# Kernel tuning notes

Measured on AMD Instinct MI355X. Metric: run time of the kernel, lower is better.

Reference implementation:

```python
import jax, jax.numpy as jnp
from jax import lax
import numpy as np

EPS = 1e-7          # BCE clamp
SMOOTH = 1.0        # Dice smoothing
INT_INF = jnp.int32(2**31 - 1)


def _bce_dice(p, t):
    """BCE + Dice loss (standard BCEDiceLoss): p, t float32 in [0,1]."""
    pc = jnp.clip(p, EPS, 1.0 - EPS)
    bce = -jnp.mean(t * jnp.log(pc) + (1.0 - t) * jnp.log1p(-pc))
    inter = jnp.sum(p * t)
    dice = 1.0 - (2.0 * inter + SMOOTH) / (jnp.sum(p) + jnp.sum(t) + SMOOTH)
    return bce + dice


def _ccl(mask):
    """4-connected component labeling per batch image.
    mask: [B,H,W] bool. Returns (labels, init_labels) int32; 0 = background.
    Iterative min-label propagation to a fixpoint (lax.while_loop)."""
    B, H, W = mask.shape
    init = jnp.where(mask, jnp.arange(1, B * H * W + 1, dtype=jnp.int32).reshape(B, H, W), 0)

    def step(lab):
        big = jnp.where(mask, lab, INT_INF)
        pad_h = jnp.full((B, 1, W), INT_INF, jnp.int32)
        pad_w = jnp.full((B, H, 1), INT_INF, jnp.int32)
        up    = jnp.concatenate([big[:, 1:, :], pad_h], axis=1)
        down  = jnp.concatenate([pad_h, big[:, :-1, :]], axis=1)
        left  = jnp.concatenate([big[:, :, 1:], pad_w], axis=2)
        right = jnp.concatenate([pad_w, big[:, :, :-1]], axis=2)
        m = jnp.minimum(big, jnp.minimum(jnp.minimum(up, down), jnp.minimum(left, right)))
        return jnp.where(mask, m, 0)

    def cond(c):
        return c[1]

    def body(c):
        new = step(c[0])
        return (new, jnp.any(new != c[0]))

    lab, _ = lax.while_loop(cond, body, (init, jnp.array(True)))
    return lab, init


def _forward(pred_out, target_mask, num_target_classes):
    f32 = jnp.float32
    B, C, H, W = pred_out.shape
    pred_masks = jnp.argmax(pred_out, axis=1)      # [B,H,W] int
    tm = target_mask[:, 0]                         # [B,H,W] int

    # background-vs-background BCEDice term
    res = _bce_dice((pred_masks == 0).astype(f32), (tm == 0).astype(f32))

    ph = jnp.zeros((B, H, W), f32)    # pred_placeholder
    pho = jnp.zeros((B, H, W), f32)   # pred_placeholder_out
    last_i = jnp.int32(1)

    # fixed loop over predicted classes (torch loops over unique values;
    # here: loop 1..C-1 gated by presence so absent classes are no-ops)
    for v in range(1, C):
        cur = pred_masks == v                       # class-v mask
        present = jnp.any(cur)
        lab, init = _ccl(cur)
        # number of connected components = pixels that kept their seed label
        n_comp = jnp.sum((lab == init) & cur).astype(jnp.int32)
        has_bg = jnp.any(~cur).astype(jnp.int32)    # 0 in cur_uniq?
        # sum_c (c_mask + last_i) over components == cur + n_comp*last_i everywhere
        inc = cur.astype(f32) + (n_comp * last_i).astype(f32)
        ph = jnp.where(present, ph + inc, ph)
        pho = jnp.where(cur, pred_out[:, v], pho)
        last_i = last_i + jnp.where(present, n_comp + has_bg, 0)

    # loop over nonzero target ids (bounded by num_target_classes), gated by presence
    for t in range(1, num_target_classes):
        target_m = tm == t
        present = jnp.any(target_m)
        n = jnp.sum(target_m)
        # torch.median(ph[target_m]): lower median of masked values
        vals = jnp.where(target_m.reshape(-1), ph.reshape(-1), jnp.inf)
        med = jnp.sort(vals)[jnp.maximum((n - 1) // 2, 0)]
        tm_f = target_m.astype(f32)
        contrib = _bce_dice(pho * (ph == med).astype(f32), tm_f)
        extra = jnp.sum(pho * ((ph != med) & target_m).astype(f32)) / jnp.maximum(n, 1).astype(f32)
        res = res + jnp.where(present, contrib + extra, 0.0)

    # len(torch.unique(target_mask)) with values in [0, num_target_classes)
    n_unique = jnp.sum(jnp.stack([jnp.any(tm == t) for t in range(num_target_classes)]).astype(jnp.int32))
    return res / (2 * n_unique + 1).astype(f32)


def setup_inputs() -> dict:
    key = jax.random.key(0)
    k1, k2 = jax.random.split(key)
    B, C, H, W = 8, 5, 768, 768
    pred_out = jax.random.uniform(k1, (B, C, H, W), dtype=jnp.float32)
    target_mask = jax.random.randint(k2, (B, 1, H, W), 0, 4, dtype=jnp.int32)
    return {"pred_out": pred_out, "target_mask": target_mask, "num_target_classes": 4}


def reference(pred_out, target_mask, num_target_classes):
    return _forward(pred_out, target_mask, num_target_classes)
```

## Files before the change

kernel.cpp:

```cpp
#include <hip/hip_runtime.h>
#include <stdint.h>
#include <math.h>

#define B_ 8
#define C_ 5
#define H_ 768
#define W_ 768
#define HW_ (H_*W_)
#define HWq (HW_/4)
#define NPIX (B_*HW_)
#define TB 8
#define INVAL 0xFFFFFFFFu
#define LN2F 0.69314718056f
#define BIASF 16.2f
#define TILE 32
#define TPR 24
#define TPC 24
#define NTILES (B_*TPR*TPC)
#define NPT 128
#define NNODES (NTILES*NPT)
#define SEAMS_PER_IMG (23*768)
#define NB_HALF (B_*SEAMS_PER_IMG)
#define NB_TOT (2*NB_HALF)
#define SEAMBLK (NB_TOT/256)
#define NCOPY 32

typedef unsigned long long ull;

static __device__ __forceinline__ unsigned pload(const unsigned* P, unsigned i) {
  return __hip_atomic_load(&P[i], __ATOMIC_RELAXED, __HIP_MEMORY_SCOPE_AGENT);
}
static __device__ unsigned findRootG(unsigned* P, unsigned i) {
  unsigned p = pload(P, i);
  if (p == i) return i;
  unsigned gp = pload(P, p);
  while (p != gp) {
    __hip_atomic_store(&P[i], gp, __ATOMIC_RELAXED, __HIP_MEMORY_SCOPE_AGENT);
    i = p; p = gp; gp = pload(P, p);
  }
  return p;
}
static __device__ bool uniteG(unsigned* P, unsigned a, unsigned b) {
  a = findRootG(P, a);
  b = findRootG(P, b);
  while (a != b) {
    if (a < b) { unsigned t = a; a = b; b = t; }
    unsigned old = atomicCAS(&P[a], a, b);
    if (old == a) return true;
    a = findRootG(P, old);
    b = findRootG(P, b);
  }
  return false;
}
static __device__ __forceinline__ unsigned ploadL(const unsigned* P, unsigned i) {
  return __hip_atomic_load(&P[i], __ATOMIC_RELAXED, __HIP_MEMORY_SCOPE_WORKGROUP);
}
static __device__ unsigned findRootL(const unsigned* P, unsigned i) {
  unsigned p = ploadL(P, i) & 0xFFFFu;
  while (p != i) { i = p; p = ploadL(P, i) & 0xFFFFu; }
  return i;
}
static __device__ void uniteL(unsigned* P, unsigned a, unsigned b) {
  a = findRootL(P, a);
  b = findRootL(P, b);
  while (a != b) {
    if (a < b) { unsigned t = a; a = b; b = t; }
    unsigned old = atomicCAS(&P[a], 0xFFFF0000u | a, 0xFFFF0000u | b);
    if (old == (0xFFFF0000u | a)) return;
    a = findRootL(P, old & 0xFFFFu);
    b = findRootL(P, b);
  }
}

__global__ __launch_bounds__(256, 8) void k_stats_ccl(
    const float* __restrict__ pred, const int* __restrict__ tgt,
    unsigned short* __restrict__ border, unsigned* __restrict__ P2,
    unsigned* __restrict__ rootcnt, double* __restrict__ sp,
    unsigned* __restrict__ ctrl)
{
  __shared__ ull h[NCOPY][41];
  __shared__ unsigned lab[TILE*TILE];
  __shared__ unsigned lclsw[TILE*TILE/4];
  __shared__ unsigned s_rt[4];
  unsigned char* lcls = (unsigned char*)lclsw;

  for (int i = threadIdx.x; i < NCOPY*41; i += 256) (&h[0][0])[i] = 0ull;
  if (threadIdx.x < 4) s_rt[threadIdx.x] = 0u;
  if (threadIdx.x < NPT) {
    unsigned n = (unsigned)blockIdx.x * NPT + threadIdx.x;
    P2[n] = n;
  }
  if (blockIdx.x == 0 && threadIdx.x == 0) ctrl[8] = 0u;
  __syncthreads();

  const int cp = threadIdx.x & (NCOPY - 1);
  int blk = blockIdx.x;
  int b = blk / (TPR*TPC);
  int rem = blk - b * (TPR*TPC);
  int trow = rem / TPR;
  int ty0 = trow * TILE;
  int tx0 = (rem - trow * TPR) * TILE;

  unsigned pk = 0u;
  {
    const int baseq = ty0 * (W_/4) + (tx0 >> 2);
    const int qrow = threadIdx.x >> 3, qcol = threadIdx.x & 7;
    const int o = qrow * (W_/4) + qcol;
    const float4* pp = (const float4*)pred + (size_t)b * (C_*HWq) + baseq + o;
    float4 a0 = pp[0];
    float4 a1 = pp[HWq];
    float4 a2 = pp[2*HWq];
    float4 a3 = pp[3*HWq];
    float4 a4 = pp[4*HWq];
    int4 t4 = ((const int4*)tgt)[(size_t)b * HWq + baseq + o];
#pragma unroll
    for (int j = 0; j < 4; ++j) {
      float v0 = ((const float*)&a0)[j];
      float v1 = ((const float*)&a1)[j];
      float v2 = ((const float*)&a2)[j];
      float v3 = ((const float*)&a3)[j];
      float v4 = ((const float*)&a4)[j];
      int tt = ((const int*)&t4)[j];
      float best = v0; int bc = 0;
      if (v1 > best) { best = v1; bc = 1; }
      if (v2 > best) { best = v2; bc = 2; }
      if (v3 > best) { best = v3; bc = 3; }
      if (v4 > best) { best = v4; bc = 4; }
      unsigned tu = (unsigned)tt; if (tu >= TB) tu = TB - 1;
      ull w;
      if (bc) {
        float pc = fminf(fmaxf(best, 1e-7f), 1.0f - 1e-7f);
        float l2p = __log2f(pc);
        float l2m = __log2f(1.0f - pc);
        float logit = (l2p - l2m) * LN2F;
        float mag   = -l2m * LN2F;
        w = (1ull << 57)
          | ((ull)__float2uint_rn(best * 4096.0f) << 38)
          | ((ull)__float2uint_rn((logit + BIASF) * 64.0f) << 20)
          | (ull)__float2uint_rn(mag * 64.0f);
      } else {
        w = 1ull << 57;
      }
      atomicAdd(&h[cp][(int)tu * C_ + bc], w);
      pk |= ((unsigned)bc) << (8 * j);
    }
    lclsw[threadIdx.x] = pk;
  }
  __syncthreads();

  const int r = threadIdx.x >> 3, sub = threadIdx.x & 7;
  const int seg = r * TILE + sub * 4;
  unsigned Dw = (r < TILE-1) ? lclsw[threadIdx.x + 8] : 0u;
  unsigned rb = (sub < 7) ? (lclsw[threadIdx.x + 1] & 255u) : 0u;
  {
    uint4 lw;
    unsigned* lp = (unsigned*)&lw;
#pragma unroll
    for (int k = 0; k < 4; ++k) {
      int li = seg + k;
      unsigned c = (pk >> (8 * k)) & 255u;
      lp[k] = c ? (0xFFFF0000u | (unsigned)li) : INVAL;
    }
    *(uint4*)&lab[seg] = lw;
  }
  __syncthreads();

#pragma unroll
  for (int j = 0; j < 4; ++j) {
    unsigned c = (pk >> (8 * j)) & 255u;
    if (!c) continue;
    int li = seg + j;
    unsigned cr = (j < 3) ? ((pk >> (8 * (j + 1))) & 255u) : rb;
    if (cr == c) uniteL(lab, li, li + 1);
    if (((Dw >> (8 * j)) & 255u) == c) uniteL(lab, li, li + TILE);
  }
  __syncthreads();

  {
    uint4 lw = *(const uint4*)&lab[seg];
    const unsigned* lp = (const unsigned*)&lw;
#pragma unroll
    for (int k = 0; k < 4; ++k) {
      int li = seg + k;
      unsigned c = (pk >> (8 * k)) & 255u;
      if (c && (lp[k] & 0xFFFFu) == (unsigned)li) atomicAdd(&s_rt[c - 1], 1u);
    }
  }
  unsigned bc_c = 0, bc_rt = 0;
  if (threadIdx.x < NPT) {
    int bp = threadIdx.x;
    int tx, ty;
    if (bp < 32)       { ty = 0;       tx = bp; }
    else if (bp < 64)  { ty = TILE-1;  tx = bp - 32; }
    else if (bp < 96)  { tx = 0;       ty = bp - 64; }
    else               { tx = TILE-1;  ty = bp - 96; }
    int li = ty * TILE + tx;
    bc_c = lcls[li];
    if (bc_c) {
      bc_rt = findRootL(lab, (unsigned)li);
      atomicMin(&lab[bc_rt], ((unsigned)threadIdx.x << 16) | bc_rt);
    }
  }
  __syncthreads();
  if (threadIdx.x < NPT) {
    unsigned sub2 = bc_c ? (lab[bc_rt] >> 16) : 0u;
    border[blk * NPT + threadIdx.x] = (unsigned short)((bc_c << 8) | sub2);
  }
  if (threadIdx.x < 4) rootcnt[blk * 4 + threadIdx.x] = s_rt[threadIdx.x];
  if (threadIdx.x < 160) {
    int slot = threadIdx.x >> 2, comp = threadIdx.x & 3;
    double s = 0.0;
#pragma unroll
    for (int cc = 0; cc < NCOPY; ++cc) {
      ull w = h[cc][slot];
      if (comp == 0)      s += (double)(w >> 57);
      else if (comp == 1) s += (double)((w >> 38) & 0x7FFFFull) * (1.0/4096.0);
      else if (comp == 2) s += (double)((w >> 20) & 0x3FFFFull) * (1.0/64.0);
      else                s += (double)(w & 0x1FFFFull) * (1.0/64.0);
    }
    sp[(size_t)blk * 160 + threadIdx.x] = s;
  }
}

#define SH_CNT(t,c)   shist[((t)*C_+(c))*4 + 0]
#define SH_PRED(t,c)  shist[((t)*C_+(c))*4 + 1]
#define SH_LRAW(t,c)  shist[((t)*C_+(c))*4 + 2]
#define SH_MAG(t,c)   shist[((t)*C_+(c))*4 + 3]
__global__ __launch_bounds__(256) void k_seam_final(
    const unsigned short* __restrict__ border, unsigned* __restrict__ P2,
    const double* __restrict__ sp, const unsigned* __restrict__ rootcnt,
    unsigned* __restrict__ smcnt, ull* __restrict__ spf_u,
    unsigned* __restrict__ ctrl, const int* __restrict__ ntcp,
    float* __restrict__ out)
{
  __shared__ unsigned s_sub[4];
  __shared__ double red[256];
  __shared__ int s_last;
  __shared__ double shist[160];
  __shared__ double s_col[C_][3];
  __shared__ unsigned s_cnti[TB*C_];
  __shared__ unsigned s_ctot[C_];
  __shared__ unsigned s_nc[4], s_smg[4];
  __shared__ float s_ph[C_];
  __shared__ double s_term[TB];
  __shared__ int s_NT;
  __shared__ int s_nun;

  if (threadIdx.x < 4) s_sub[threadIdx.x] = 0u;
  __syncthreads();
  int idx = blockIdx.x * blockDim.x + threadIdx.x;
  {
    int tA, tB, pA, pB;
    if (idx < NB_HALF) {
      int b = idx / SEAMS_PER_IMG;
      int r = idx - b * SEAMS_PER_IMG;
      int seam = r / W_;
      int x = r - seam * W_;
      int tj = x >> 5, k = x & 31;
      tA = (b * TPC + seam) * TPR + tj;
      tB = tA + TPR;
      pA = tA * NPT + 32 + k;
      pB = tB * NPT + 0 + k;
    } else {
      int i2 = idx - NB_HALF;
      int b = i2 / SEAMS_PER_IMG;
      int r = i2 - b * SEAMS_PER_IMG;
      int seam = r / H_;
      int y = r - seam * H_;
      int ti = y >> 5, k = y & 31;
      tA = (b * TPC + ti) * TPR + seam;
      tB = tA + 1;
      pA = tA * NPT + 96 + k;
      pB = tB * NPT + 64 + k;
    }
    unsigned a16 = border[pA];
    unsigned b16 = border[pB];
    unsigned ca = a16 >> 8, cb = b16 >> 8;
    if (ca && ca == cb) {
      if (uniteG(P2, (unsigned)tA * NPT + (a16 & 255u),
                     (unsigned)tB * NPT + (b16 & 255u)))
        atomicAdd(&s_sub[ca - 1], 1u);
    }
  }
  if (blockIdx.x < 160) {
    double s = 0.0;
    for (int j = threadIdx.x; j < NTILES; j += 256) s += sp[(size_t)j * 160 + blockIdx.x];
    red[threadIdx.x] = s;
    __syncthreads();
    for (int off = 128; off; off >>= 1) {
      if (threadIdx.x < off) red[threadIdx.x] += red[threadIdx.x + off];
      __syncthreads();
    }
    if (threadIdx.x == 0)
      __hip_atomic_store(&spf_u[blockIdx.x], (ull)__double_as_longlong(red[0]),
                         __ATOMIC_RELAXED, __HIP_MEMORY_SCOPE_AGENT);
  }
  __syncthreads();
  if (threadIdx.x < 4)
    __hip_atomic_store(&smcnt[blockIdx.x * 4 + threadIdx.x], s_sub[threadIdx.x],
                       __ATOMIC_RELAXED, __HIP_MEMORY_SCOPE_AGENT);
  __syncthreads();
  if (threadIdx.x == 0) {
    unsigned old = __hip_atomic_fetch_add(&ctrl[8], 1u,
                     __ATOMIC_RELAXED, __HIP_MEMORY_SCOPE_AGENT);
    s_last = (old == (unsigned)(SEAMBLK - 1));
  }
  __syncthreads();
  if (!s_last) return;

  if (threadIdx.x < 160) {
    ull u = __hip_atomic_load(&spf_u[threadIdx.x],
              __ATOMIC_RELAXED, __HIP_MEMORY_SCOPE_AGENT);
    shist[threadIdx.x] = __longlong_as_double((long long)u);
  }
  if (threadIdx.x < 4) { s_nc[threadIdx.x] = 0u; s_smg[threadIdx.x] = 0u; }
  if (threadIdx.x < TB) s_term[threadIdx.x] = 0.0;
  if (threadIdx.x == 0) {
    int NT = ntcp[0];
    if (NT < 1) NT = 1;
    if (NT > TB) NT = TB;
    s_NT = NT;
  }
  __syncthreads();
  {
    unsigned a = 0;
    for (int j = threadIdx.x; j < NTILES * 4; j += 256) a += rootcnt[j];
    if (a) atomicAdd(&s_nc[threadIdx.x & 3], a);
  }
  {
    unsigned a = 0;
    for (int j = threadIdx.x; j < SEAMBLK * 4; j += 256)
      a += __hip_atomic_load(&smcnt[j], __ATOMIC_RELAXED, __HIP_MEMORY_SCOPE_AGENT);
    if (a) atomicAdd(&s_smg[threadIdx.x & 3], a);
  }
  __syncthreads();

  if (threadIdx.x < TB * C_) s_cnti[threadIdx.x] = (unsigned)llrint(shist[threadIdx.x * 4]);
  __syncthreads();

  if (threadIdx.x < C_) {
    int c = threadIdx.x;
    double sc = 0.0, sp2 = 0.0, sl = 0.0;
    unsigned ct = 0;
#pragma unroll
    for (int t = 0; t < TB; ++t) {
      sc += SH_CNT(t, c);
      sp2 += SH_PRED(t, c);
      sl += -SH_MAG(t, c);
      ct += s_cnti[t * C_ + c];
    }
    s_col[c][0] = sc; s_col[c][1] = sp2; s_col[c][2] = sl;
    s_ctot[c] = ct;
  }
  __syncthreads();

  if (threadIdx.x == 0) {
#pragma unroll
    for (int cc = 0; cc < C_; ++cc) {
      float ph = 0.0f;
      int li = 1;
#pragma unroll
      for (int v = 1; v < C_; ++v) {
        unsigned ncv = s_nc[v - 1] - s_smg[v - 1];
        if (s_ctot[v] > 0) {
          int prod = (int)(ncv * (unsigned)li);
          float sv = (float)prod;
          float inc = ((cc == v) ? 1.0f : 0.0f) + sv;
          ph = ph + inc;
          li = li + (int)ncv + ((s_ctot[v] < (unsigned)NPIX) ? 1 : 0);
        }
      }
      s_ph[cc] = ph;
    }
  }
  __syncthreads();

  const float EPSF = 1e-7f;
  const double L1 = (double)logf(1.0f - EPSF);
  const double M1 = (double)log1pf(-(1.0f - EPSF));
  const double L0 = (double)logf(EPSF);
  const double M0 = (double)log1pf(-EPSF);
  const double N = (double)NPIX;
  const double BIASD = (double)BIASF;
  const int NT = s_NT;

  if (threadIdx.x == 0) {
    double nt0 = 0;
#pragma unroll
    for (int c = 0; c < C_; ++c) nt0 += SH_CNT(0, c);
    double np1 = (double)s_ctot[0];
    double n11 = SH_CNT(0, 0);
    s_term[0] = -(n11*L1 + (nt0 - n11)*L0 + (np1 - n11)*M1 + (N - nt0 - np1 + n11)*M0) / N
                + 1.0 - (2.0*n11 + 1.0) / (np1 + nt0 + 1.0);
    int nun = 0;
    for (int t = 0; t < NT; ++t) {
      long long s = 0;
#pragma unroll
      for (int c = 0; c < C_; ++c) s += (long long)s_cnti[t * C_ + c];
      if (s) nun++;
    }
    s_nun = nun;
  } else if (threadIdx.x < (unsigned)NT) {
    int t = threadIdx.x;
    long long ntti = 0;
#pragma unroll
    for (int c = 0; c < C_; ++c) ntti += (long long)s_cnti[t * C_ + c];
    if (ntti != 0) {
      double ntt = 0;
#pragma unroll
      for (int c = 0; c < C_; ++c) ntt += SH_CNT(t, c);
      float pht[C_] = {s_ph[0], s_ph[1], s_ph[2], s_ph[3], s_ph[4]};
      int idx2[C_] = {0, 1, 2, 3, 4};
#pragma unroll
      for (int i = 1; i < C_; ++i)
        for (int j = i; j > 0 && pht[idx2[j]] < pht[idx2[j-1]]; --j) {
          int tmp = idx2[j]; idx2[j] = idx2[j-1]; idx2[j-1] = tmp;
        }
      long long k = (ntti - 1) / 2;
      float med = pht[idx2[C_ - 1]];
      long long cum = 0;
#pragma unroll
      for (int i = 0; i < C_; ++i) {
        cum += (long long)s_cnti[t * C_ + idx2[i]];
        if (cum > k) { med = pht[idx2[i]]; break; }
      }
      double A = 0, Bt = 0, inter = 0, sum_p = 0, ex = 0, nfg_t = 0, nfg_all = 0;
#pragma unroll
      for (int c = 1; c < C_; ++c) {
        double cnt_tc = SH_CNT(t, c);
        double mag_tc = SH_MAG(t, c);
        double spred_tc = SH_PRED(t, c);
        if (pht[c] == med) {
          double logit = SH_LRAW(t, c) - BIASD * cnt_tc;
          A += logit - mag_tc;
          inter += spred_tc;
          nfg_t += cnt_tc;
          nfg_all += s_col[c][0];
          sum_p += s_col[c][1];
          Bt += s_col[c][2] - (-mag_tc);
        } else {
          ex += spred_tc;
        }
      }
      double bce  = -(A + Bt + (ntt - nfg_t)*L0 + (N - ntt - (nfg_all - nfg_t))*M0) / N;
      double dice = 1.0 - (2.0*inter + 1.0) / (sum_p + ntt + 1.0);
      s_term[t] = bce + dice + ex / ntt;
    }
  }
  __syncthreads();
  if (threadIdx.x == 0) {
    double res = 0.0;
#pragma unroll
    for (int t = 0; t < TB; ++t) res += s_term[t];
    out[0] = (float)(res / (double)(2 * s_nun + 1));
  }
}

extern "C" void kernel_launch(void* const* d_in, const int* in_sizes, int n_in,
                              void* d_out, int out_size, void* d_ws, size_t ws_size,
                              hipStream_t stream) {
  const float* pred = (const float*)d_in[0];
  const int* tgt = (const int*)d_in[1];
  const int* ntc = (const int*)d_in[2];
  float* out = (float*)d_out;
  char* ws = (char*)d_ws;
  size_t off = 0;
  unsigned* ctrl = (unsigned*)(ws + off);        off += 16 * 4;
  ull* spf_u = (ull*)(ws + off);                 off += 160 * 8;
  double* sp = (double*)(ws + off);              off += (size_t)NTILES * 160 * 8;
  unsigned* P2 = (unsigned*)(ws + off);          off += (size_t)NNODES * 4;
  unsigned short* border = (unsigned short*)(ws + off); off += (size_t)NTILES * NPT * 2;
  unsigned* rootcnt = (unsigned*)(ws + off);     off += (size_t)NTILES * 4 * 4;
  unsigned* smcnt = (unsigned*)(ws + off);       off += (size_t)SEAMBLK * 4 * 4;

  hipLaunchKernelGGL(k_stats_ccl, dim3(NTILES), dim3(256), 0, stream,
                     pred, tgt, border, P2, rootcnt, sp, ctrl);
  hipLaunchKernelGGL(k_seam_final, dim3(SEAMBLK), dim3(256), 0, stream,
                     border, P2, sp, rootcnt, smcnt, spf_u, ctrl, ntc, out);
}
```

Baseline: 211.4 us.

## Replace per-tile partial-sum arrays with replicated global atomics and a separate final kernel

Per-tile double partial statistics (NTILES×160 doubles) and per-tile root counts are no longer written and later reduced. Each tile now does fixed-point integer atomic adds into a small replicated global accumulator. The seam kernel likewise atomically adds its counts into replicas, and a new single-block final kernel sums the replicas and resets them. This drops a large write-then-read reduction and the last-block detection, in exchange for atomic contention, a third kernel launch, and reliance on device globals being reset at the end of each call. NCOPY is also halved, which shrinks shared histogram memory.

After: 172.2 us. 18.5% less time.

```diff
diff --git a/kernel.cpp b/kernel.cpp
--- a/kernel.cpp
+++ b/kernel.cpp
@@ -23,9 +23,14 @@
 #define NB_HALF (B_*SEAMS_PER_IMG)
 #define NB_TOT (2*NB_HALF)
 #define SEAMBLK (NB_TOT/256)
-#define NCOPY 32
+#define NCOPY 16
+#define REPS 8
+#define REPC 64
 
 typedef unsigned long long ull;
+
+__device__ ull g_spu[REPS * 160];
+__device__ unsigned g_crep[REPC * 16];
 
 static __device__ __forceinline__ unsigned pload(const unsigned* P, unsigned i) {
   return __hip_atomic_load(&P[i], __ATOMIC_RELAXED, __HIP_MEMORY_SCOPE_AGENT);
@@ -74,9 +79,7 @@
 
 __global__ __launch_bounds__(256, 8) void k_stats_ccl(
     const float* __restrict__ pred, const int* __restrict__ tgt,
-    unsigned short* __restrict__ border, unsigned* __restrict__ P2,
-    unsigned* __restrict__ rootcnt, double* __restrict__ sp,
-    unsigned* __restrict__ ctrl)
+    unsigned short* __restrict__ border, unsigned* __restrict__ P2)
 {
   __shared__ ull h[NCOPY][41];
   __shared__ unsigned lab[TILE*TILE];
@@ -90,7 +93,6 @@
     unsigned n = (unsigned)blockIdx.x * NPT + threadIdx.x;
     P2[n] = n;
   }
-  if (blockIdx.x == 0 && threadIdx.x == 0) ctrl[8] = 0u;
   __syncthreads();
 
   const int cp = threadIdx.x & (NCOPY - 1);
@@ -206,46 +208,27 @@
     unsigned sub2 = bc_c ? (lab[bc_rt] >> 16) : 0u;
     border[blk * NPT + threadIdx.x] = (unsigned short)((bc_c << 8) | sub2);
   }
-  if (threadIdx.x < 4) rootcnt[blk * 4 + threadIdx.x] = s_rt[threadIdx.x];
+  if (threadIdx.x < 4 && s_rt[threadIdx.x])
+    atomicAdd(&g_crep[(blk & (REPC-1)) * 16 + threadIdx.x], s_rt[threadIdx.x]);
   if (threadIdx.x < 160) {
     int slot = threadIdx.x >> 2, comp = threadIdx.x & 3;
-    double s = 0.0;
+    ull fs = 0;
 #pragma unroll
     for (int cc = 0; cc < NCOPY; ++cc) {
       ull w = h[cc][slot];
-      if (comp == 0)      s += (double)(w >> 57);
-      else if (comp == 1) s += (double)((w >> 38) & 0x7FFFFull) * (1.0/4096.0);
-      else if (comp == 2) s += (double)((w >> 20) & 0x3FFFFull) * (1.0/64.0);
-      else                s += (double)(w & 0x1FFFFull) * (1.0/64.0);
-    }
-    sp[(size_t)blk * 160 + threadIdx.x] = s;
-  }
-}
-
-#define SH_CNT(t,c)   shist[((t)*C_+(c))*4 + 0]
-#define SH_PRED(t,c)  shist[((t)*C_+(c))*4 + 1]
-#define SH_LRAW(t,c)  shist[((t)*C_+(c))*4 + 2]
-#define SH_MAG(t,c)   shist[((t)*C_+(c))*4 + 3]
-__global__ __launch_bounds__(256) void k_seam_final(
-    const unsigned short* __restrict__ border, unsigned* __restrict__ P2,
-    const double* __restrict__ sp, const unsigned* __restrict__ rootcnt,
-    unsigned* __restrict__ smcnt, ull* __restrict__ spf_u,
-    unsigned* __restrict__ ctrl, const int* __restrict__ ntcp,
-    float* __restrict__ out)
+      if (comp == 0)      fs += (w >> 57);
+      else if (comp == 1) fs += (w >> 38) & 0x7FFFFull;
+      else if (comp == 2) fs += (w >> 20) & 0x3FFFFull;
+      else                fs += w & 0x1FFFFull;
+    }
+    if (fs) atomicAdd(&g_spu[(blk & (REPS-1)) * 160 + threadIdx.x], fs);
+  }
+}
+
+__global__ __launch_bounds__(256) void k_seam(const unsigned short* __restrict__ border,
+                                              unsigned* __restrict__ P2)
 {
   __shared__ unsigned s_sub[4];
-  __shared__ double red[256];
-  __shared__ int s_last;
-  __shared__ double shist[160];
-  __shared__ double s_col[C_][3];
-  __shared__ unsigned s_cnti[TB*C_];
-  __shared__ unsigned s_ctot[C_];
-  __shared__ unsigned s_nc[4], s_smg[4];
-  __shared__ float s_ph[C_];
-  __shared__ double s_term[TB];
-  __shared__ int s_NT;
-  __shared__ int s_nun;
-
   if (threadIdx.x < 4) s_sub[threadIdx.x] = 0u;
   __syncthreads();
   int idx = blockIdx.x * blockDim.x + threadIdx.x;
@@ -282,56 +265,49 @@
         atomicAdd(&s_sub[ca - 1], 1u);
     }
   }
-  if (blockIdx.x < 160) {
-    double s = 0.0;
-    for (int j = threadIdx.x; j < NTILES; j += 256) s += sp[(size_t)j * 160 + blockIdx.x];
-    red[threadIdx.x] = s;
-    __syncthreads();
-    for (int off = 128; off; off >>= 1) {
-      if (threadIdx.x < off) red[threadIdx.x] += red[threadIdx.x + off];
-      __syncthreads();
-    }
-    if (threadIdx.x == 0)
-      __hip_atomic_store(&spf_u[blockIdx.x], (ull)__double_as_longlong(red[0]),
-                         __ATOMIC_RELAXED, __HIP_MEMORY_SCOPE_AGENT);
-  }
-  __syncthreads();
-  if (threadIdx.x < 4)
-    __hip_atomic_store(&smcnt[blockIdx.x * 4 + threadIdx.x], s_sub[threadIdx.x],
-                       __ATOMIC_RELAXED, __HIP_MEMORY_SCOPE_AGENT);
-  __syncthreads();
-  if (threadIdx.x == 0) {
-    unsigned old = __hip_atomic_fetch_add(&ctrl[8], 1u,
-                     __ATOMIC_RELAXED, __HIP_MEMORY_SCOPE_AGENT);
-    s_last = (old == (unsigned)(SEAMBLK - 1));
-  }
-  __syncthreads();
-  if (!s_last) return;
+  __syncthreads();
+  if (threadIdx.x < 4 && s_sub[threadIdx.x])
+    atomicAdd(&g_crep[(blockIdx.x & (REPC-1)) * 16 + 4 + threadIdx.x], s_sub[threadIdx.x]);
+}
+
+#define SH_CNT(t,c)   shist[((t)*C_+(c))*4 + 0]
+#define SH_PRED(t,c)  shist[((t)*C_+(c))*4 + 1]
+#define SH_LRAW(t,c)  shist[((t)*C_+(c))*4 + 2]
+#define SH_MAG(t,c)   shist[((t)*C_+(c))*4 + 3]
+__global__ __launch_bounds__(256) void k_final(const int* __restrict__ ntcp,
+                                               float* __restrict__ out)
+{
+  __shared__ double shist[160];
+  __shared__ double s_col[C_][3];
+  __shared__ unsigned s_cnti[TB*C_];
+  __shared__ unsigned s_ctot[C_];
+  __shared__ unsigned s_nc[4], s_smg[4];
+  __shared__ float s_ph[C_];
+  __shared__ double s_term[TB];
+  __shared__ int s_NT;
+  __shared__ int s_nun;
 
   if (threadIdx.x < 160) {
-    ull u = __hip_atomic_load(&spf_u[threadIdx.x],
-              __ATOMIC_RELAXED, __HIP_MEMORY_SCOPE_AGENT);
-    shist[threadIdx.x] = __longlong_as_double((long long)u);
-  }
-  if (threadIdx.x < 4) { s_nc[threadIdx.x] = 0u; s_smg[threadIdx.x] = 0u; }
+    ull acc = 0;
+#pragma unroll
+    for (int rp = 0; rp < REPS; ++rp) acc += g_spu[rp * 160 + threadIdx.x];
+    int comp = threadIdx.x & 3;
+    shist[threadIdx.x] = (comp == 0) ? (double)acc
+                       : (comp == 1) ? (double)acc * (1.0/4096.0)
+                                     : (double)acc * (1.0/64.0);
+  }
+  if (threadIdx.x < 8) {
+    unsigned a = 0;
+    for (int rp = 0; rp < REPC; ++rp) a += g_crep[rp * 16 + threadIdx.x];
+    if (threadIdx.x < 4) s_nc[threadIdx.x] = a;
+    else                 s_smg[threadIdx.x - 4] = a;
+  }
   if (threadIdx.x < TB) s_term[threadIdx.x] = 0.0;
   if (threadIdx.x == 0) {
     int NT = ntcp[0];
     if (NT < 1) NT = 1;
     if (NT > TB) NT = TB;
     s_NT = NT;
-  }
-  __syncthreads();
-  {
-    unsigned a = 0;
-    for (int j = threadIdx.x; j < NTILES * 4; j += 256) a += rootcnt[j];
-    if (a) atomicAdd(&s_nc[threadIdx.x & 3], a);
-  }
-  {
-    unsigned a = 0;
-    for (int j = threadIdx.x; j < SEAMBLK * 4; j += 256)
-      a += __hip_atomic_load(&smcnt[j], __ATOMIC_RELAXED, __HIP_MEMORY_SCOPE_AGENT);
-    if (a) atomicAdd(&s_smg[threadIdx.x & 3], a);
   }
   __syncthreads();
 
@@ -454,6 +430,9 @@
     for (int t = 0; t < TB; ++t) res += s_term[t];
     out[0] = (float)(res / (double)(2 * s_nun + 1));
   }
+  __syncthreads();
+  for (int i = threadIdx.x; i < REPS * 160; i += 256) g_spu[i] = 0ull;
+  for (int i = threadIdx.x; i < REPC * 16; i += 256) g_crep[i] = 0u;
 }
 
 extern "C" void kernel_launch(void* const* d_in, const int* in_sizes, int n_in,
@@ -465,16 +444,11 @@
   float* out = (float*)d_out;
   char* ws = (char*)d_ws;
   size_t off = 0;
-  unsigned* ctrl = (unsigned*)(ws + off);        off += 16 * 4;
-  ull* spf_u = (ull*)(ws + off);                 off += 160 * 8;
-  double* sp = (double*)(ws + off);              off += (size_t)NTILES * 160 * 8;
   unsigned* P2 = (unsigned*)(ws + off);          off += (size_t)NNODES * 4;
   unsigned short* border = (unsigned short*)(ws + off); off += (size_t)NTILES * NPT * 2;
-  unsigned* rootcnt = (unsigned*)(ws + off);     off += (size_t)NTILES * 4 * 4;
-  unsigned* smcnt = (unsigned*)(ws + off);       off += (size_t)SEAMBLK * 4 * 4;
 
   hipLaunchKernelGGL(k_stats_ccl, dim3(NTILES), dim3(256), 0, stream,
-                     pred, tgt, border, P2, rootcnt, sp, ctrl);
-  hipLaunchKernelGGL(k_seam_final, dim3(SEAMBLK), dim3(256), 0, stream,
-                     border, P2, sp, rootcnt, smcnt, spf_u, ctrl, ntc, out);
-}
+                     pred, tgt, border, P2);
+  hipLaunchKernelGGL(k_seam, dim3(SEAMBLK), dim3(256), 0, stream, border, P2);
+  hipLaunchKernelGGL(k_final, dim3(1), dim3(256), 0, stream, ntc, out);
+}
```
